# Kernel tuning notes

Measured on AMD Instinct MI355X. Metric: run time of the kernel, lower is better.

Reference implementation:

```python
import jax, jax.numpy as jnp
import numpy as np

N_ATOMS = 100000
N_BONDS = 2000000
F = 32  # fixed feature width implied by hardcoded MLP input dims


def _linear_init(key, din, dout):
    kw, kb = jax.random.split(key)
    s = 1.0 / np.sqrt(din)
    w = jax.random.uniform(kw, (din, dout), jnp.float32, -s, s)
    b = jax.random.uniform(kb, (dout,), jnp.float32, -s, s)
    return w, b


def _mlp(x, w1, b1, w2, b2, w3, b3):
    # Linear(din,64)-SELU-Linear(64,64)-SELU-Linear(64,32)-SELU
    x = jax.nn.selu(x @ w1 + b1)
    x = jax.nn.selu(x @ w2 + b2)
    return jax.nn.selu(x @ w3 + b3)


def setup_inputs() -> dict:
    key = jax.random.key(0)
    ks = jax.random.split(key, 14)
    inp = {
        "bonds": jax.random.normal(ks[0], (N_BONDS, F), jnp.float32),
        "bond_atom_1": jax.random.randint(ks[1], (N_BONDS,), 0, N_ATOMS, jnp.int32),
        "bond_atom_2": jax.random.randint(ks[2], (N_BONDS,), 0, N_ATOMS, jnp.int32),
        "atoms": jax.random.normal(ks[3], (N_ATOMS, F), jnp.float32),
        "state": jax.random.normal(ks[4], (1, F), jnp.float32),
    }
    # phi_e: 128 -> 64 -> 64 -> 32
    inp["e_w1"], inp["e_b1"] = _linear_init(ks[5], 128, 64)
    inp["e_w2"], inp["e_b2"] = _linear_init(ks[6], 64, 64)
    inp["e_w3"], inp["e_b3"] = _linear_init(ks[7], 64, 32)
    # phi_v: 96 -> 64 -> 64 -> 32
    inp["v_w1"], inp["v_b1"] = _linear_init(ks[8], 96, 64)
    inp["v_w2"], inp["v_b2"] = _linear_init(ks[9], 64, 64)
    inp["v_w3"], inp["v_b3"] = _linear_init(ks[10], 64, 32)
    # phi_u: 96 -> 64 -> 64 -> 32
    inp["u_w1"], inp["u_b1"] = _linear_init(ks[11], 96, 64)
    inp["u_w2"], inp["u_b2"] = _linear_init(ks[12], 64, 64)
    inp["u_w3"], inp["u_b3"] = _linear_init(ks[13], 64, 32)
    return inp


def reference(bonds, bond_atom_1, bond_atom_2, atoms, state,
              e_w1, e_b1, e_w2, e_b2, e_w3, e_b3,
              v_w1, v_b1, v_w2, v_b2, v_w3, v_b3,
              u_w1, u_b1, u_w2, u_b2, u_w3, u_b3):
    n_bonds = bonds.shape[0]
    n_atoms = atoms.shape[0]
    state_b = jnp.broadcast_to(state, (n_bonds, state.shape[1]))
    # gather atom features per bond endpoint
    a1 = atoms[bond_atom_1]  # [E, F]
    a2 = atoms[bond_atom_2]  # [E, F]
    bonds_new = _mlp(jnp.concatenate([a1, a2, bonds, state_b], axis=1),
                     e_w1, e_b1, e_w2, e_b2, e_w3, e_b3)  # [E, 32]
    # scatter-add bond messages back to atom 1, normalize by bond count
    b2a = jax.ops.segment_sum(bonds_new, bond_atom_1, num_segments=n_atoms)  # [N, 32]
    cnt = jax.ops.segment_sum(jnp.ones((n_bonds,), bonds_new.dtype), bond_atom_1,
                              num_segments=n_atoms)  # [N]
    b2a = b2a / cnt[:, None]
    state_a = jnp.broadcast_to(state, (n_atoms, state.shape[1]))
    atoms_new = _mlp(jnp.concatenate([b2a, atoms, state_a], axis=1),
                     v_w1, v_b1, v_w2, v_b2, v_w3, v_b3)  # [N, 32]
    state_new = _mlp(jnp.concatenate([jnp.mean(bonds_new, axis=0, keepdims=True),
                                      jnp.mean(atoms_new, axis=0, keepdims=True),
                                      state], axis=1),
                     u_w1, u_b1, u_w2, u_b2, u_w3, u_b3)  # [1, 32]
    return bonds_new, atoms_new, state_new
```

## Files before the change

kernel.cpp:

```cpp
#include <hip/hip_runtime.h>
#include <math.h>

typedef __attribute__((ext_vector_type(4))) int    int4v;
typedef __attribute__((ext_vector_type(4))) float  float4v;
typedef __attribute__((ext_vector_type(8))) __bf16 bf16x8;

#define SCAN_BLK 1024
#define EBLK 512

static constexpr float SELU_SCALE = 1.0507009873554805f;
static constexpr float SELU_ALPHA = 1.6732632423543772f;

__device__ __forceinline__ float selu_f(float x) {
    const float sa = SELU_SCALE * SELU_ALPHA;
    float e = __expf(x);
    return x > 0.0f ? SELU_SCALE * x : fmaf(sa, e, -sa);
}

__device__ __forceinline__ unsigned short f2bf(float f) {
    uint32_t u = __builtin_bit_cast(uint32_t, f);
    return (unsigned short)((u + 0x7FFFu + ((u >> 16) & 1u)) >> 16);
}

__device__ __forceinline__ uint32_t pk2(float a, float b) {
    uint32_t r;
    asm("v_cvt_pk_bf16_f32 %0, %1, %2" : "=v"(r) : "v"(a), "v"(b));
    return r;
}

__device__ __forceinline__ float4v mfma_bf16(int4v a, int4v b, float4v c) {
    return __builtin_amdgcn_mfma_f32_16x16x32_bf16(
        __builtin_bit_cast(bf16x8, a), __builtin_bit_cast(bf16x8, b), c, 0, 0, 0);
}


__global__ __launch_bounds__(256) void cnt_kernel(const int* __restrict__ ba1,
                                                  int* __restrict__ cnt, int nb) {
    for (int e = blockIdx.x * 256 + threadIdx.x; e < nb; e += gridDim.x * 256)
        atomicAdd(cnt + ba1[e], 1);
}

__global__ __launch_bounds__(SCAN_BLK) void scan_block_kernel(const int* __restrict__ cnt,
                                                              int* __restrict__ excl,
                                                              int* __restrict__ bsums, int na) {
    __shared__ int tmp[SCAN_BLK];
    const int t = threadIdx.x;
    const int base = blockIdx.x * SCAN_BLK;
    const int v = (base + t < na) ? cnt[base + t] : 0;
    tmp[t] = v;
    __syncthreads();
    for (int off = 1; off < SCAN_BLK; off <<= 1) {
        const int add = (t >= off) ? tmp[t - off] : 0;
        __syncthreads();
        tmp[t] += add;
        __syncthreads();
    }
    if (base + t < na) excl[base + t] = tmp[t] - v;
    if (t == SCAN_BLK - 1) bsums[blockIdx.x] = tmp[t];
}

__global__ __launch_bounds__(128) void scan_tops_kernel(const int* __restrict__ bsums,
                                                        int* __restrict__ bases, int nblocks) {
    __shared__ int tmp[128];
    const int t = threadIdx.x;
    const int v = (t < nblocks) ? bsums[t] : 0;
    tmp[t] = v;
    __syncthreads();
    for (int off = 1; off < 128; off <<= 1) {
        const int add = (t >= off) ? tmp[t - off] : 0;
        __syncthreads();
        tmp[t] += add;
        __syncthreads();
    }
    if (t < nblocks) bases[t] = tmp[t] - v;
}

__global__ __launch_bounds__(256) void wcur_init_kernel(const int* __restrict__ excl,
                                                        const int* __restrict__ bases,
                                                        int* __restrict__ wcur, int na) {
    const int a = blockIdx.x * 256 + threadIdx.x;
    if (a < na) wcur[a] = bases[a >> 10] + excl[a];
}


__global__ void bias_prep_kernel(const float* __restrict__ state,
                                 const float* __restrict__ ew1, const float* __restrict__ eb1,
                                 const float* __restrict__ vw1, const float* __restrict__ vb1,
                                 float* __restrict__ ebias, float* __restrict__ vbias) {
    const int t = threadIdx.x;
    if (t >= 64) return;
    if (blockIdx.x == 0) {
        float acc = eb1[t];
        for (int k = 0; k < 32; ++k) acc = fmaf(state[k], ew1[(96 + k) * 64 + t], acc);
        ebias[t] = acc;
    } else {
        float acc = vb1[t];
        for (int k = 0; k < 32; ++k) acc = fmaf(state[k], vw1[(64 + k) * 64 + t], acc);
        vbias[t] = acc;
    }
}


__global__ __launch_bounds__(256) void aprep_kernel(const float* __restrict__ atoms,
                                                    unsigned short* __restrict__ abf,
                                                    int nel8) {
    const int i = blockIdx.x * 256 + threadIdx.x;
    if (i >= nel8) return;
    const float* p = atoms + (size_t)i * 8;
    uint4 v;
    v.x = pk2(p[0], p[1]); v.y = pk2(p[2], p[3]);
    v.z = pk2(p[4], p[5]); v.w = pk2(p[6], p[7]);
    *(uint4*)(abf + (size_t)i * 8) = v;
}

__global__ __launch_bounds__(256) void wprep_kernel(
    const float* __restrict__ ew1, const float* __restrict__ ew2, const float* __restrict__ ew3,
    const float* __restrict__ vw1, const float* __restrict__ vw2, const float* __restrict__ vw3,
    unsigned short* __restrict__ wfe, unsigned short* __restrict__ wfv)
{
    const int idx = blockIdx.x * 256 + threadIdx.x;
    if (idx >= 44 * 64) return;
    const int fid = idx >> 6, lane = idx & 63;
    const int b = lane & 15, g = lane >> 4;
    const float* W; int N, t, c;
    if (fid < 12)      { W = ew1; N = 64; t = fid / 3;        c = fid % 3; }
    else if (fid < 20) { W = ew2; N = 64; t = (fid - 12) / 2; c = (fid - 12) % 2; }
    else if (fid < 24) { W = ew3; N = 32; t = (fid - 20) / 2; c = (fid - 20) % 2; }
    else if (fid < 32) { W = vw1; N = 64; t = (fid - 24) / 2; c = (fid - 24) % 2; }
    else if (fid < 40) { W = vw2; N = 64; t = (fid - 32) / 2; c = (fid - 32) % 2; }
    else               { W = vw3; N = 32; t = (fid - 40) / 2; c = (fid - 40) % 2; }
    unsigned short* dst = (fid < 24) ? (wfe + fid * 512) : (wfv + (fid - 24) * 512);
    for (int j = 0; j < 8; ++j) {
        const float w = W[(size_t)(32 * c + 8 * g + j) * N + 16 * t + b];
        dst[lane * 8 + j] = f2bf(w);
    }
}


__global__ __launch_bounds__(EBLK, 8) void phi_e_mfma(
    const float* __restrict__ bonds, const int* __restrict__ ba1, const int* __restrict__ ba2,
    const unsigned short* __restrict__ abf,
    const unsigned short* __restrict__ wfe, const float* __restrict__ ebias,
    const float* __restrict__ eb2, const float* __restrict__ eb3,
    float* __restrict__ out, int* __restrict__ wcur, int* __restrict__ list, int nb)
{
    __shared__ __align__(16) char lds[25344 + (EBLK / 64) * 2048];
    {
        const uint4* src = (const uint4*)wfe;
        uint4* dst = (uint4*)lds;
        #pragma unroll
        for (int i = 0; i < 3; ++i) dst[threadIdx.x + i * EBLK] = src[threadIdx.x + i * EBLK];
        float* bd = (float*)(lds + 24576);
        const int t = threadIdx.x;
        if (t < 64)        bd[t] = ebias[t];
        else if (t < 128)  bd[t] = eb2[t - 64];
        else if (t < 160)  bd[t] = eb3[t - 128];
    }
    __syncthreads();

    const char* wl = lds;
    const float* bias_l = (const float*)(lds + 24576);
    const int tid = threadIdx.x;
    const int wid = tid >> 6, lane = tid & 63;
    const int b = lane & 15, g = lane >> 4;
    char* hb = lds + 25344 + wid * 2048;
    const uint32_t swz = (uint32_t)((b & 7) << 4);
    const uint32_t row = (uint32_t)(b * 128);
    const uint32_t loff = (uint32_t)(lane * 16);

    const int ntile = (nb + 15) >> 4;
    const int stride = gridDim.x * (EBLK / 64);

    for (int m = blockIdx.x * (EBLK / 64) + wid; m < ntile; m += stride) {
        const int e0 = m << 4;
        const int er = min(e0 + b, nb - 1);
        const int i1 = ba1[er], i2 = ba2[er];

        if (lane < 16 && e0 + b < nb) {
            const int pos = atomicAdd(wcur + i1, 1);
            __builtin_nontemporal_store(er, list + pos);
        }

        const int4v xa1 = *(const int4v*)(abf + (size_t)i1 * 32 + 8 * g);
        const int4v xa2 = *(const int4v*)(abf + (size_t)i2 * 32 + 8 * g);
        int4v xb;
        {
            const float* p = bonds + (size_t)er * 32 + 8 * g;
            const float4v u0 = __builtin_nontemporal_load((const float4v*)p);
            const float4v u1 = __builtin_nontemporal_load((const float4v*)p + 1);
            xb[0] = (int)pk2(u0.x, u0.y); xb[1] = (int)pk2(u0.z, u0.w);
            xb[2] = (int)pk2(u1.x, u1.y); xb[3] = (int)pk2(u1.z, u1.w);
        }

        float4v acc[4];
        #pragma unroll
        for (int t = 0; t < 4; ++t) acc[t] = *(const float4v*)(bias_l + 16 * t + 4 * g);
        #pragma unroll
        for (int t = 0; t < 4; ++t) {
            acc[t] = mfma_bf16(*(const int4v*)(wl + (t * 3 + 0) * 1024 + loff), xa1, acc[t]);
            acc[t] = mfma_bf16(*(const int4v*)(wl + (t * 3 + 1) * 1024 + loff), xa2, acc[t]);
            acc[t] = mfma_bf16(*(const int4v*)(wl + (t * 3 + 2) * 1024 + loff), xb,  acc[t]);
        }
        #pragma unroll
        for (int t = 0; t < 4; ++t) {
            const float s0 = selu_f(acc[t][0]), s1 = selu_f(acc[t][1]);
            const float s2 = selu_f(acc[t][2]), s3 = selu_f(acc[t][3]);
            const uint32_t q = (uint32_t)(t * 32 + g * 8);
            *(uint2*)(hb + row + (q ^ swz)) = make_uint2(pk2(s0, s1), pk2(s2, s3));
        }
        int4v xh0 = *(const int4v*)(hb + row + (((uint32_t)(g * 16)) ^ swz));
        int4v xh1 = *(const int4v*)(hb + row + (((uint32_t)(64 + g * 16)) ^ swz));

        #pragma unroll
        for (int t = 0; t < 4; ++t) acc[t] = *(const float4v*)(bias_l + 64 + 16 * t + 4 * g);
        #pragma unroll
        for (int t = 0; t < 4; ++t) {
            acc[t] = mfma_bf16(*(const int4v*)(wl + (12 + t * 2 + 0) * 1024 + loff), xh0, acc[t]);
            acc[t] = mfma_bf16(*(const int4v*)(wl + (12 + t * 2 + 1) * 1024 + loff), xh1, acc[t]);
        }
        #pragma unroll
        for (int t = 0; t < 4; ++t) {
            const float s0 = selu_f(acc[t][0]), s1 = selu_f(acc[t][1]);
            const float s2 = selu_f(acc[t][2]), s3 = selu_f(acc[t][3]);
            const uint32_t q = (uint32_t)(t * 32 + g * 8);
            *(uint2*)(hb + row + (q ^ swz)) = make_uint2(pk2(s0, s1), pk2(s2, s3));
        }
        xh0 = *(const int4v*)(hb + row + (((uint32_t)(g * 16)) ^ swz));
        xh1 = *(const int4v*)(hb + row + (((uint32_t)(64 + g * 16)) ^ swz));

        float4v acc3[2];
        acc3[0] = *(const float4v*)(bias_l + 128 + 4 * g);
        acc3[1] = *(const float4v*)(bias_l + 128 + 16 + 4 * g);
        #pragma unroll
        for (int t = 0; t < 2; ++t) {
            acc3[t] = mfma_bf16(*(const int4v*)(wl + (20 + t * 2 + 0) * 1024 + loff), xh0, acc3[t]);
            acc3[t] = mfma_bf16(*(const int4v*)(wl + (20 + t * 2 + 1) * 1024 + loff), xh1, acc3[t]);
        }
        if (e0 + b < nb) {
            #pragma unroll
            for (int t = 0; t < 2; ++t) {
                float4v ov;
                ov.x = selu_f(acc3[t][0]); ov.y = selu_f(acc3[t][1]);
                ov.z = selu_f(acc3[t][2]); ov.w = selu_f(acc3[t][3]);
                *(float4v*)(out + (size_t)(e0 + b) * 32 + 16 * t + 4 * g) = ov;
            }
        }
    }
}


__global__ __launch_bounds__(256) void gather_mean_kernel(
    const float* __restrict__ bonds_new, const int* __restrict__ list,
    const int* __restrict__ excl, const int* __restrict__ bases,
    const int* __restrict__ cnt, float* __restrict__ mean,
    float* __restrict__ bpart, int na)
{
    __shared__ float red[4][32];
    const int idx = blockIdx.x * 256 + threadIdx.x;
    const int a = idx >> 3, q = idx & 7;
    float4v sv[8];
    #pragma unroll
    for (int i = 0; i < 8; ++i) sv[i] = (float4v){0.f, 0.f, 0.f, 0.f};
    int n = 0;
    if (a < na) {
        const int start = bases[a >> 10] + excl[a];
        n = cnt[a];
        const int end = start + n;
        int p = start;
        for (; p + 8 <= end; p += 8) {
            int e[8];
            #pragma unroll
            for (int i = 0; i < 8; ++i) e[i] = list[p + i];
            #pragma unroll
            for (int i = 0; i < 8; ++i)
                sv[i] += *(const float4v*)(bonds_new + (size_t)e[i] * 32 + q * 4);
        }
        for (; p + 2 <= end; p += 2) {
            const int e0 = list[p], e1 = list[p + 1];
            sv[0] += *(const float4v*)(bonds_new + (size_t)e0 * 32 + q * 4);
            sv[1] += *(const float4v*)(bonds_new + (size_t)e1 * 32 + q * 4);
        }
        if (p < end)
            sv[0] += *(const float4v*)(bonds_new + (size_t)list[p] * 32 + q * 4);
    }
    float4v s = ((sv[0] + sv[1]) + (sv[2] + sv[3])) + ((sv[4] + sv[5]) + (sv[6] + sv[7]));

    {
        float4v t = s;
        #pragma unroll
        for (int off = 8; off < 64; off <<= 1) {
            t.x += __shfl_xor(t.x, off); t.y += __shfl_xor(t.y, off);
            t.z += __shfl_xor(t.z, off); t.w += __shfl_xor(t.w, off);
        }
        const int wv = threadIdx.x >> 6;
        const int lane = threadIdx.x & 63;
        if (lane < 8) {
            red[wv][lane * 4 + 0] = t.x; red[wv][lane * 4 + 1] = t.y;
            red[wv][lane * 4 + 2] = t.z; red[wv][lane * 4 + 3] = t.w;
        }
        __syncthreads();
        if (threadIdx.x < 32) {
            const int f = threadIdx.x;
            bpart[(size_t)blockIdx.x * 32 + f] =
                red[0][f] + red[1][f] + red[2][f] + red[3][f];
        }
    }

    if (a < na) {
        const float inv = 1.0f / (float)n;
        *(float4v*)(mean + (size_t)a * 32 + q * 4) = s * inv;
    }
}


__global__ __launch_bounds__(1024) void part_reduce_kernel(const float* __restrict__ part,
                                                           float* __restrict__ dst, int nblk) {
    __shared__ float red[32][33];
    const int f = threadIdx.x & 31;
    const int c = threadIdx.x >> 5;
    float s = 0.0f;
    for (int i = c; i < nblk; i += 32) s += part[(size_t)i * 32 + f];
    red[c][f] = s;
    __syncthreads();
    if (threadIdx.x < 32) {
        float t = 0.0f;
        #pragma unroll
        for (int c2 = 0; c2 < 32; ++c2) t += red[c2][threadIdx.x];
        dst[threadIdx.x] = t;
    }
}


__global__ __launch_bounds__(256) void phi_v_mfma(
    const unsigned short* __restrict__ abf, float* __restrict__ out ,
    const unsigned short* __restrict__ wfv, const float* __restrict__ vbias,
    const float* __restrict__ vb2, const float* __restrict__ vb3,
    float* __restrict__ apart, int na)
{
    __shared__ __align__(16) char lds_raw[4 * 2048];
    __shared__ float redv[4][32];
    const int tid = threadIdx.x;
    const int wid = tid >> 6, lane = tid & 63;
    const int b = lane & 15, g = lane >> 4;
    char* hb = lds_raw + wid * 2048;
    const uint32_t swz = (uint32_t)((b & 7) << 4);
    const uint32_t row = (uint32_t)(b * 128);

    int4v wv1[4][2], wv2[4][2], wv3[2][2];
    #pragma unroll
    for (int t = 0; t < 4; ++t)
        #pragma unroll
        for (int c = 0; c < 2; ++c) {
            wv1[t][c] = *(const int4v*)(wfv + (t * 2 + c) * 512 + lane * 8);
            wv2[t][c] = *(const int4v*)(wfv + (8 + t * 2 + c) * 512 + lane * 8);
        }
    #pragma unroll
    for (int t = 0; t < 2; ++t)
        #pragma unroll
        for (int c = 0; c < 2; ++c)
            wv3[t][c] = *(const int4v*)(wfv + (16 + t * 2 + c) * 512 + lane * 8);

    float ssum[8];
    #pragma unroll
    for (int i = 0; i < 8; ++i) ssum[i] = 0.0f;

    const int ntile = (na + 15) >> 4;
    const int m = blockIdx.x * 4 + wid;
    if (m < ntile) {
        const int a0 = m << 4;
        const int ar = (a0 + b < na) ? (a0 + b) : (na - 1);

        int4v xm;
        {
            const float* p = out + (size_t)ar * 32 + 8 * g;
            const float4v u0 = *(const float4v*)p, u1 = *(const float4v*)(p + 4);
            xm[0] = (int)pk2(u0.x, u0.y); xm[1] = (int)pk2(u0.z, u0.w);
            xm[2] = (int)pk2(u1.x, u1.y); xm[3] = (int)pk2(u1.z, u1.w);
        }
        const int4v xa = *(const int4v*)(abf + (size_t)ar * 32 + 8 * g);

        float4v acc[4];
        #pragma unroll
        for (int t = 0; t < 4; ++t) acc[t] = *(const float4v*)(vbias + 16 * t + 4 * g);
        #pragma unroll
        for (int t = 0; t < 4; ++t) {
            acc[t] = mfma_bf16(wv1[t][0], xm, acc[t]);
            acc[t] = mfma_bf16(wv1[t][1], xa, acc[t]);
        }
        #pragma unroll
        for (int t = 0; t < 4; ++t) {
            const float s0 = selu_f(acc[t][0]), s1 = selu_f(acc[t][1]);
            const float s2 = selu_f(acc[t][2]), s3 = selu_f(acc[t][3]);
            const uint32_t q = (uint32_t)(t * 32 + g * 8);
            *(uint2*)(hb + row + (q ^ swz)) = make_uint2(pk2(s0, s1), pk2(s2, s3));
        }
        int4v xh0 = *(const int4v*)(hb + row + (((uint32_t)(g * 16)) ^ swz));
        int4v xh1 = *(const int4v*)(hb + row + (((uint32_t)(64 + g * 16)) ^ swz));

        #pragma unroll
        for (int t = 0; t < 4; ++t) acc[t] = *(const float4v*)(vb2 + 16 * t + 4 * g);
        #pragma unroll
        for (int t = 0; t < 4; ++t) {
            acc[t] = mfma_bf16(wv2[t][0], xh0, acc[t]);
            acc[t] = mfma_bf16(wv2[t][1], xh1, acc[t]);
        }
        #pragma unroll
        for (int t = 0; t < 4; ++t) {
            const float s0 = selu_f(acc[t][0]), s1 = selu_f(acc[t][1]);
            const float s2 = selu_f(acc[t][2]), s3 = selu_f(acc[t][3]);
            const uint32_t q = (uint32_t)(t * 32 + g * 8);
            *(uint2*)(hb + row + (q ^ swz)) = make_uint2(pk2(s0, s1), pk2(s2, s3));
        }
        xh0 = *(const int4v*)(hb + row + (((uint32_t)(g * 16)) ^ swz));
        xh1 = *(const int4v*)(hb + row + (((uint32_t)(64 + g * 16)) ^ swz));

        float4v acc3[2];
        acc3[0] = *(const float4v*)(vb3 + 4 * g);
        acc3[1] = *(const float4v*)(vb3 + 16 + 4 * g);
        #pragma unroll
        for (int t = 0; t < 2; ++t) {
            acc3[t] = mfma_bf16(wv3[t][0], xh0, acc3[t]);
            acc3[t] = mfma_bf16(wv3[t][1], xh1, acc3[t]);
        }
        if (a0 + b < na) {
            #pragma unroll
            for (int t = 0; t < 2; ++t) {
                const float o0 = selu_f(acc3[t][0]), o1 = selu_f(acc3[t][1]);
                const float o2 = selu_f(acc3[t][2]), o3 = selu_f(acc3[t][3]);
                float4v ov; ov.x = o0; ov.y = o1; ov.z = o2; ov.w = o3;
                *(float4v*)(out + (size_t)(a0 + b) * 32 + 16 * t + 4 * g) = ov;
                ssum[t * 4 + 0] += o0; ssum[t * 4 + 1] += o1;
                ssum[t * 4 + 2] += o2; ssum[t * 4 + 3] += o3;
            }
        }
    }

    #pragma unroll
    for (int i = 0; i < 8; ++i) {
        float v = ssum[i];
        v += __shfl_xor(v, 1); v += __shfl_xor(v, 2);
        v += __shfl_xor(v, 4); v += __shfl_xor(v, 8);
        if (b == 0) redv[wid][16 * (i >> 2) + 4 * g + (i & 3)] = v;
    }
    __syncthreads();
    if (tid < 32)
        apart[(size_t)blockIdx.x * 32 + tid] =
            redv[0][tid] + redv[1][tid] + redv[2][tid] + redv[3][tid];
}


__global__ __launch_bounds__(128) void phi_u_kernel(
    const float* __restrict__ bsum, const float* __restrict__ asum,
    const float* __restrict__ state,
    const float* __restrict__ w1, const float* __restrict__ b1,
    const float* __restrict__ w2, const float* __restrict__ b2,
    const float* __restrict__ w3, const float* __restrict__ b3,
    float* __restrict__ out, float inv_nb, float inv_na)
{
    __shared__ float x[96];
    __shared__ float hs[64];
    const int t = threadIdx.x;
    if (t < 32)       x[t] = bsum[t] * inv_nb;
    else if (t < 64)  x[t] = asum[t - 32] * inv_na;
    else if (t < 96)  x[t] = state[t - 64];
    __syncthreads();
    if (t < 64) {
        float acc = b1[t];
        for (int k = 0; k < 96; ++k) acc = fmaf(x[k], w1[k * 64 + t], acc);
        hs[t] = selu_f(acc);
    }
    __syncthreads();
    float acc2 = 0.0f;
    if (t < 64) {
        acc2 = b2[t];
        for (int k = 0; k < 64; ++k) acc2 = fmaf(hs[k], w2[k * 64 + t], acc2);
        acc2 = selu_f(acc2);
    }
    __syncthreads();
    if (t < 64) hs[t] = acc2;
    __syncthreads();
    if (t < 32) {
        float acc = b3[t];
        for (int k = 0; k < 64; ++k) acc = fmaf(hs[k], w3[k * 32 + t], acc);
        out[t] = selu_f(acc);
    }
}

extern "C" void kernel_launch(void* const* d_in, const int* in_sizes, int n_in,
                              void* d_out, int out_size, void* d_ws, size_t ws_size,
                              hipStream_t stream) {
    const float* bonds = (const float*)d_in[0];
    const int*   ba1   = (const int*)d_in[1];
    const int*   ba2   = (const int*)d_in[2];
    const float* atoms = (const float*)d_in[3];
    const float* state = (const float*)d_in[4];
    const float* ew1 = (const float*)d_in[5];  const float* eb1 = (const float*)d_in[6];
    const float* ew2 = (const float*)d_in[7];  const float* eb2 = (const float*)d_in[8];
    const float* ew3 = (const float*)d_in[9];  const float* eb3 = (const float*)d_in[10];
    const float* vw1 = (const float*)d_in[11]; const float* vb1 = (const float*)d_in[12];
    const float* vw2 = (const float*)d_in[13]; const float* vb2 = (const float*)d_in[14];
    const float* vw3 = (const float*)d_in[15]; const float* vb3 = (const float*)d_in[16];
    const float* uw1 = (const float*)d_in[17]; const float* ub1 = (const float*)d_in[18];
    const float* uw2 = (const float*)d_in[19]; const float* ub2 = (const float*)d_in[20];
    const float* uw3 = (const float*)d_in[21]; const float* ub3 = (const float*)d_in[22];

    const int nb = in_sizes[1];
    const int na = in_sizes[3] / 32;
    const int nscan = (na + SCAN_BLK - 1) / SCAN_BLK;
    const int ngather = ((na * 8) + 255) / 256;
    const int ntv = (na + 15) / 16;
    const int nvblk = (ntv + 3) / 4;

    float* out       = (float*)d_out;
    float* bonds_out = out;
    float* atoms_out = out + (size_t)nb * 32;
    float* state_out = atoms_out + (size_t)na * 32;

    char* ws = (char*)d_ws;
    size_t off = 0;
    auto alloc = [&](size_t bytes) { char* p = ws + off; off += (bytes + 255) & ~(size_t)255; return p; };
    int*   cnt   = (int*)alloc((size_t)na * 4);
    const size_t zero_bytes = off;
    float* bsum  = (float*)alloc(32 * 4);
    float* asum  = (float*)alloc(32 * 4);
    float* ebias = (float*)alloc(64 * 4);
    float* vbias = (float*)alloc(64 * 4);
    int*   excl  = (int*)alloc((size_t)na * 4);
    int*   bsums = (int*)alloc(128 * 4);
    int*   bases = (int*)alloc(128 * 4);
    int*   wcur  = (int*)alloc((size_t)na * 4);
    int*   list  = (int*)alloc((size_t)nb * 4);
    float* bpart = (float*)alloc((size_t)ngather * 32 * 4);
    float* apart = (float*)alloc((size_t)nvblk * 32 * 4);
    unsigned short* wfe = (unsigned short*)alloc(24 * 512 * 2);
    unsigned short* wfv = (unsigned short*)alloc(20 * 512 * 2);
    unsigned short* abf = (unsigned short*)alloc((size_t)na * 32 * 2);

    (void)hipMemsetAsync(d_ws, 0, zero_bytes, stream);

    bias_prep_kernel<<<2, 64, 0, stream>>>(state, ew1, eb1, vw1, vb1, ebias, vbias);
    wprep_kernel<<<(44 * 64 + 255) / 256, 256, 0, stream>>>(ew1, ew2, ew3, vw1, vw2, vw3,
                                                            wfe, wfv);
    aprep_kernel<<<(na * 4 + 255) / 256, 256, 0, stream>>>(atoms, abf, na * 4);

    cnt_kernel<<<2048, 256, 0, stream>>>(ba1, cnt, nb);
    scan_block_kernel<<<nscan, SCAN_BLK, 0, stream>>>(cnt, excl, bsums, na);
    scan_tops_kernel<<<1, 128, 0, stream>>>(bsums, bases, nscan);
    wcur_init_kernel<<<(na + 255) / 256, 256, 0, stream>>>(excl, bases, wcur, na);

    phi_e_mfma<<<1024, EBLK, 0, stream>>>(bonds, ba1, ba2, abf, wfe, ebias, eb2, eb3,
                                          bonds_out, wcur, list, nb);

    gather_mean_kernel<<<ngather, 256, 0, stream>>>(bonds_out, list, excl, bases, cnt,
                                                    atoms_out, bpart, na);
    part_reduce_kernel<<<1, 1024, 0, stream>>>(bpart, bsum, ngather);

    phi_v_mfma<<<nvblk, 256, 0, stream>>>(abf, atoms_out, wfv, vbias, vb2, vb3,
                                          apart, na);
    part_reduce_kernel<<<1, 1024, 0, stream>>>(apart, asum, nvblk);

    phi_u_kernel<<<1, 128, 0, stream>>>(bsum, asum, state,
                                        uw1, ub1, uw2, ub2, uw3, ub3,
                                        state_out, 1.0f / (float)nb, 1.0f / (float)na);
}
```

Measured before the change: 437.0 us.

## Process two bond tiles per wave iteration and merge prep kernels

Each wave in the edge MLP kernel now handles a pair of 16-bond tiles. All gathers and bond loads for both tiles are issued before the MLP runs, which raises memory-level parallelism and hides gather latency. The occupancy hint in launch bounds drops from 8 to 4 waves-per-EU to leave room for the extra registers. The three small prep kernels (bias, weight-fragment, atom bf16 conversion) are merged into one launch to cut launch overhead, at the cost of lower occupancy in the edge kernel.

```diff
diff --git a/kernel.cpp b/kernel.cpp
--- a/kernel.cpp
+++ b/kernel.cpp
@@ -83,17 +83,45 @@
 }
 
 
-__global__ void bias_prep_kernel(const float* __restrict__ state,
-                                 const float* __restrict__ ew1, const float* __restrict__ eb1,
-                                 const float* __restrict__ vw1, const float* __restrict__ vb1,
-                                 float* __restrict__ ebias, float* __restrict__ vbias) {
-    const int t = threadIdx.x;
-    if (t >= 64) return;
-    if (blockIdx.x == 0) {
-        float acc = eb1[t];
-        for (int k = 0; k < 32; ++k) acc = fmaf(state[k], ew1[(96 + k) * 64 + t], acc);
-        ebias[t] = acc;
-    } else {
+__global__ __launch_bounds__(256) void prep_all_kernel(
+    const float* __restrict__ atoms, unsigned short* __restrict__ abf, int nel8,
+    const float* __restrict__ ew1, const float* __restrict__ ew2, const float* __restrict__ ew3,
+    const float* __restrict__ vw1, const float* __restrict__ vw2, const float* __restrict__ vw3,
+    unsigned short* __restrict__ wfe, unsigned short* __restrict__ wfv,
+    const float* __restrict__ state,
+    const float* __restrict__ eb1, const float* __restrict__ vb1,
+    float* __restrict__ ebias, float* __restrict__ vbias)
+{
+    const int i = blockIdx.x * 256 + threadIdx.x;
+    if (i < nel8) {
+        const float* p = atoms + (size_t)i * 8;
+        uint4 v;
+        v.x = pk2(p[0], p[1]); v.y = pk2(p[2], p[3]);
+        v.z = pk2(p[4], p[5]); v.w = pk2(p[6], p[7]);
+        *(uint4*)(abf + (size_t)i * 8) = v;
+    }
+    if (i < 44 * 64) {
+        const int fid = i >> 6, lane = i & 63;
+        const int b = lane & 15, g = lane >> 4;
+        const float* W; int N, t, c;
+        if (fid < 12)      { W = ew1; N = 64; t = fid / 3;        c = fid % 3; }
+        else if (fid < 20) { W = ew2; N = 64; t = (fid - 12) / 2; c = (fid - 12) % 2; }
+        else if (fid < 24) { W = ew3; N = 32; t = (fid - 20) / 2; c = (fid - 20) % 2; }
+        else if (fid < 32) { W = vw1; N = 64; t = (fid - 24) / 2; c = (fid - 24) % 2; }
+        else if (fid < 40) { W = vw2; N = 64; t = (fid - 32) / 2; c = (fid - 32) % 2; }
+        else               { W = vw3; N = 32; t = (fid - 40) / 2; c = (fid - 40) % 2; }
+        unsigned short* dst = (fid < 24) ? (wfe + fid * 512) : (wfv + (fid - 24) * 512);
+        for (int j = 0; j < 8; ++j) {
+            const float w = W[(size_t)(32 * c + 8 * g + j) * N + 16 * t + b];
+            dst[lane * 8 + j] = f2bf(w);
+        }
+    }
+    if (i < 64) {
+        float acc = eb1[i];
+        for (int k = 0; k < 32; ++k) acc = fmaf(state[k], ew1[(96 + k) * 64 + i], acc);
+        ebias[i] = acc;
+    } else if (i < 128) {
+        const int t = i - 64;
         float acc = vb1[t];
         for (int k = 0; k < 32; ++k) acc = fmaf(state[k], vw1[(64 + k) * 64 + t], acc);
         vbias[t] = acc;
@@ -101,43 +129,7 @@
 }
 
 
-__global__ __launch_bounds__(256) void aprep_kernel(const float* __restrict__ atoms,
-                                                    unsigned short* __restrict__ abf,
-                                                    int nel8) {
-    const int i = blockIdx.x * 256 + threadIdx.x;
-    if (i >= nel8) return;
-    const float* p = atoms + (size_t)i * 8;
-    uint4 v;
-    v.x = pk2(p[0], p[1]); v.y = pk2(p[2], p[3]);
-    v.z = pk2(p[4], p[5]); v.w = pk2(p[6], p[7]);
-    *(uint4*)(abf + (size_t)i * 8) = v;
-}
-
-__global__ __launch_bounds__(256) void wprep_kernel(
-    const float* __restrict__ ew1, const float* __restrict__ ew2, const float* __restrict__ ew3,
-    const float* __restrict__ vw1, const float* __restrict__ vw2, const float* __restrict__ vw3,
-    unsigned short* __restrict__ wfe, unsigned short* __restrict__ wfv)
-{
-    const int idx = blockIdx.x * 256 + threadIdx.x;
-    if (idx >= 44 * 64) return;
-    const int fid = idx >> 6, lane = idx & 63;
-    const int b = lane & 15, g = lane >> 4;
-    const float* W; int N, t, c;
-    if (fid < 12)      { W = ew1; N = 64; t = fid / 3;        c = fid % 3; }
-    else if (fid < 20) { W = ew2; N = 64; t = (fid - 12) / 2; c = (fid - 12) % 2; }
-    else if (fid < 24) { W = ew3; N = 32; t = (fid - 20) / 2; c = (fid - 20) % 2; }
-    else if (fid < 32) { W = vw1; N = 64; t = (fid - 24) / 2; c = (fid - 24) % 2; }
-    else if (fid < 40) { W = vw2; N = 64; t = (fid - 32) / 2; c = (fid - 32) % 2; }
-    else               { W = vw3; N = 32; t = (fid - 40) / 2; c = (fid - 40) % 2; }
-    unsigned short* dst = (fid < 24) ? (wfe + fid * 512) : (wfv + (fid - 24) * 512);
-    for (int j = 0; j < 8; ++j) {
-        const float w = W[(size_t)(32 * c + 8 * g + j) * N + 16 * t + b];
-        dst[lane * 8 + j] = f2bf(w);
-    }
-}
-
-
-__global__ __launch_bounds__(EBLK, 8) void phi_e_mfma(
+__global__ __launch_bounds__(EBLK, 4) void phi_e_mfma(
     const float* __restrict__ bonds, const int* __restrict__ ba1, const int* __restrict__ ba2,
     const unsigned short* __restrict__ abf,
     const unsigned short* __restrict__ wfe, const float* __restrict__ ebias,
@@ -169,29 +161,10 @@
     const uint32_t loff = (uint32_t)(lane * 16);
 
     const int ntile = (nb + 15) >> 4;
+    const int npair = (ntile + 1) >> 1;
     const int stride = gridDim.x * (EBLK / 64);
 
-    for (int m = blockIdx.x * (EBLK / 64) + wid; m < ntile; m += stride) {
-        const int e0 = m << 4;
-        const int er = min(e0 + b, nb - 1);
-        const int i1 = ba1[er], i2 = ba2[er];
-
-        if (lane < 16 && e0 + b < nb) {
-            const int pos = atomicAdd(wcur + i1, 1);
-            __builtin_nontemporal_store(er, list + pos);
-        }
-
-        const int4v xa1 = *(const int4v*)(abf + (size_t)i1 * 32 + 8 * g);
-        const int4v xa2 = *(const int4v*)(abf + (size_t)i2 * 32 + 8 * g);
-        int4v xb;
-        {
-            const float* p = bonds + (size_t)er * 32 + 8 * g;
-            const float4v u0 = __builtin_nontemporal_load((const float4v*)p);
-            const float4v u1 = __builtin_nontemporal_load((const float4v*)p + 1);
-            xb[0] = (int)pk2(u0.x, u0.y); xb[1] = (int)pk2(u0.z, u0.w);
-            xb[2] = (int)pk2(u1.x, u1.y); xb[3] = (int)pk2(u1.z, u1.w);
-        }
-
+    auto mlp = [&](int4v xa1, int4v xa2, int4v xb, int e0) {
         float4v acc[4];
         #pragma unroll
         for (int t = 0; t < 4; ++t) acc[t] = *(const float4v*)(bias_l + 16 * t + 4 * g);
@@ -244,6 +217,52 @@
                 ov.z = selu_f(acc3[t][2]); ov.w = selu_f(acc3[t][3]);
                 *(float4v*)(out + (size_t)(e0 + b) * 32 + 16 * t + 4 * g) = ov;
             }
+        }
+    };
+
+    for (int P = blockIdx.x * (EBLK / 64) + wid; P < npair; P += stride) {
+        const int mA = P << 1;
+        const bool hasB = (mA + 1) < ntile;
+        const int e0a = mA << 4;
+        const int e0b = e0a + 16;
+        const int era = min(e0a + b, nb - 1);
+        const int erb = hasB ? min(e0b + b, nb - 1) : era;
+        const int i1a = ba1[era], i2a = ba2[era];
+        const int i1b = ba1[erb], i2b = ba2[erb];
+
+        if (lane < 16) {
+            if (e0a + b < nb) {
+                const int pos = atomicAdd(wcur + i1a, 1);
+                __builtin_nontemporal_store(era, list + pos);
+            }
+            if (hasB && e0b + b < nb) {
+                const int pos = atomicAdd(wcur + i1b, 1);
+                __builtin_nontemporal_store(erb, list + pos);
+            }
+        }
+
+        const int4v xa1a = *(const int4v*)(abf + (size_t)i1a * 32 + 8 * g);
+        const int4v xa2a = *(const int4v*)(abf + (size_t)i2a * 32 + 8 * g);
+        const float* pa = bonds + (size_t)era * 32 + 8 * g;
+        const float4v ua0 = __builtin_nontemporal_load((const float4v*)pa);
+        const float4v ua1 = __builtin_nontemporal_load((const float4v*)pa + 1);
+        const int4v xa1b = *(const int4v*)(abf + (size_t)i1b * 32 + 8 * g);
+        const int4v xa2b = *(const int4v*)(abf + (size_t)i2b * 32 + 8 * g);
+        const float* pb = bonds + (size_t)erb * 32 + 8 * g;
+        const float4v ub0 = __builtin_nontemporal_load((const float4v*)pb);
+        const float4v ub1 = __builtin_nontemporal_load((const float4v*)pb + 1);
+
+        {
+            int4v xb;
+            xb[0] = (int)pk2(ua0.x, ua0.y); xb[1] = (int)pk2(ua0.z, ua0.w);
+            xb[2] = (int)pk2(ua1.x, ua1.y); xb[3] = (int)pk2(ua1.z, ua1.w);
+            mlp(xa1a, xa2a, xb, e0a);
+        }
+        if (hasB) {
+            int4v xb;
+            xb[0] = (int)pk2(ub0.x, ub0.y); xb[1] = (int)pk2(ub0.z, ub0.w);
+            xb[2] = (int)pk2(ub1.x, ub1.y); xb[3] = (int)pk2(ub1.z, ub1.w);
+            mlp(xa1b, xa2b, xb, e0b);
         }
     }
 }
@@ -538,10 +557,9 @@
 
     (void)hipMemsetAsync(d_ws, 0, zero_bytes, stream);
 
-    bias_prep_kernel<<<2, 64, 0, stream>>>(state, ew1, eb1, vw1, vb1, ebias, vbias);
-    wprep_kernel<<<(44 * 64 + 255) / 256, 256, 0, stream>>>(ew1, ew2, ew3, vw1, vw2, vw3,
-                                                            wfe, wfv);
-    aprep_kernel<<<(na * 4 + 255) / 256, 256, 0, stream>>>(atoms, abf, na * 4);
+    prep_all_kernel<<<(na * 4 + 255) / 256, 256, 0, stream>>>(
+        atoms, abf, na * 4, ew1, ew2, ew3, vw1, vw2, vw3, wfe, wfv,
+        state, eb1, vb1, ebias, vbias);
 
     cnt_kernel<<<2048, 256, 0, stream>>>(ba1, cnt, nb);
     scan_block_kernel<<<nscan, SCAN_BLK, 0, stream>>>(cnt, excl, bsums, na);
```

Result: no change. 432.0 us (median of 2 runs) (-1.1%).
